# Performance work log

Hardware: AMD Instinct MI355X
Metric: run time of the kernel (lower is better)

## Reference

```python
import jax, jax.numpy as jnp
import numpy as np
from jax import lax

B, CIN, COUT, K, S, P, H, W = 8, 128, 256, 3, 1, 1, 64, 64


def setup_inputs() -> dict:
    key = jax.random.key(0)
    k1, k2, k3, k4, k5 = jax.random.split(key, 5)
    fan_off = CIN * K * K
    fan_dc = CIN * K * K
    return {
        "x": jax.random.normal(k1, (B, CIN, H, W), dtype=jnp.float32),
        # offset-predicting conv: Conv2d(CIN, 2*K*K, K, S, P, padding_mode='reflect')
        "w_off": jax.random.normal(k2, (2 * K * K, CIN, K, K), dtype=jnp.float32) / np.sqrt(fan_off),
        "b_off": jax.random.normal(k3, (2 * K * K,), dtype=jnp.float32) * 0.01,
        # deformable conv weights: DeformConv2d(CIN, COUT, K, S, P)
        "w_dc": jax.random.normal(k4, (COUT, CIN, K, K), dtype=jnp.float32) / np.sqrt(fan_dc),
        "b_dc": jax.random.normal(k5, (COUT,), dtype=jnp.float32) * 0.01,
    }


def _reflect_conv(x, w, b, stride, pad):
    # Conv2d with reflect padding
    xp = jnp.pad(x, ((0, 0), (0, 0), (pad, pad), (pad, pad)), mode="reflect")
    y = lax.conv_general_dilated(xp, w, (stride, stride), "VALID",
                                 dimension_numbers=("NCHW", "OIHW", "NCHW"))
    return y + b[None, :, None, None]


def _deform_conv(x, offset, w, b, k, stride, pad):
    # torchvision DeformConv2d (v1, no mask, 1 offset group)
    Bn, C, Hi, Wi = x.shape
    Ho, Wo = offset.shape[2], offset.shape[3]
    KK = k * k
    # offset layout: [B, 2*KK, Ho, Wo], interleaved (dy, dx) per kernel position
    off = offset.reshape(Bn, KK, 2, Ho, Wo)
    hb = jnp.arange(Ho, dtype=x.dtype) * stride - pad          # base rows
    wb = jnp.arange(Wo, dtype=x.dtype) * stride - pad          # base cols
    ki, kj = jnp.meshgrid(jnp.arange(k, dtype=x.dtype), jnp.arange(k, dtype=x.dtype), indexing="ij")
    ki, kj = ki.reshape(KK), kj.reshape(KK)
    # sampling locations [B, KK, Ho, Wo]
    py = off[:, :, 0] + hb[None, None, :, None] + ki[None, :, None, None]
    px = off[:, :, 1] + wb[None, None, None, :] + kj[None, :, None, None]
    y0 = jnp.floor(py)
    x0 = jnp.floor(px)
    dy = (py - y0).reshape(Bn, 1, -1)
    dx = (px - x0).reshape(Bn, 1, -1)
    y0i = y0.astype(jnp.int32)
    x0i = x0.astype(jnp.int32)
    xf = x.reshape(Bn, C, Hi * Wi)

    def gather(yi, xi):
        valid = (yi >= 0) & (yi < Hi) & (xi >= 0) & (xi < Wi)
        yc = jnp.clip(yi, 0, Hi - 1)
        xc = jnp.clip(xi, 0, Wi - 1)
        idx = (yc * Wi + xc).reshape(Bn, -1)                   # [B, KK*Ho*Wo]
        g = jax.vmap(lambda xb, ib: xb[:, ib])(xf, idx)        # [B, C, KK*Ho*Wo]
        return g * valid.reshape(Bn, 1, -1).astype(x.dtype)

    v00 = gather(y0i, x0i)
    v01 = gather(y0i, x0i + 1)
    v10 = gather(y0i + 1, x0i)
    v11 = gather(y0i + 1, x0i + 1)
    vals = (v00 * (1 - dy) * (1 - dx) + v01 * (1 - dy) * dx
            + v10 * dy * (1 - dx) + v11 * dy * dx)             # [B, C, KK*Ho*Wo]
    cols = vals.reshape(Bn, C, KK, Ho * Wo)
    out = jnp.einsum("bckl,ock->bol", cols, w.reshape(-1, C, KK))
    out = out + b[None, :, None]
    return out.reshape(Bn, -1, Ho, Wo)


def reference(x, w_off, b_off, w_dc, b_dc):
    x_offset = _reflect_conv(x, w_off, b_off, S, P)            # [B, 2*K*K, Ho, Wo]
    # torch.chunk followed by torch.concat is an identity on the offset tensor
    return _deform_conv(x, x_offset, w_dc, b_dc, K, S, P)
```

## Files before the change

### kernel.cpp

```cpp
#include <hip/hip_runtime.h>
#include <hip/hip_fp16.h>

typedef unsigned short u16;
typedef unsigned int   u32;
typedef u32   u32x2  __attribute__((ext_vector_type(2)));
typedef u32   u32x4  __attribute__((ext_vector_type(4)));
typedef short short8 __attribute__((ext_vector_type(8)));
typedef float f32x4  __attribute__((ext_vector_type(4)));
typedef _Float16 half8 __attribute__((ext_vector_type(8)));

__device__ __forceinline__ u16 f2h(float f) { return __half_as_ushort(__float2half(f)); }
__device__ __forceinline__ f32x4 mfma16(short8 a, short8 b, f32x4 c) {
  return __builtin_amdgcn_mfma_f32_16x16x32_f16(
      __builtin_bit_cast(half8, a), __builtin_bit_cast(half8, b), c, 0, 0, 0);
}
__device__ __forceinline__ __half2 h2cast(u32 u) { return __builtin_bit_cast(__half2, u); }

__global__ __launch_bounds__(256) void prep_fused(const float* __restrict__ x,
                                                  const float* __restrict__ w_dc,
                                                  const float* __restrict__ w_off,
                                                  u16* __restrict__ xh,
                                                  u16* __restrict__ Wl2,
                                                  u16* __restrict__ Wol2) {
  int bid = blockIdx.x;
  int tid = threadIdx.x;
  if (bid < 512) {
    __shared__ float tile[128][65];
    int swz = (bid & 7) * 64 + (bid >> 3);
    int b = swz >> 6, h = swz & 63;
    for (int i = 0; i < 32; ++i) {
      int c = (tid >> 6) + i * 4;
      int w = tid & 63;
      tile[c][w] = x[(((size_t)b * 128 + c) * 64 + h) * 64 + w];
    }
    __syncthreads();
    u16* dst = xh + ((size_t)(b * 64 + h) * 64) * 128;
    for (int j = 0; j < 32; ++j) {
      int c = tid & 127;
      int w = (tid >> 7) + 2 * j;
      dst[w * 128 + c] = f2h(tile[c][w]);
    }
  } else {
    int idx = (bid - 512) * 256 + tid;
    if (idx < 294912) {
      int e = idx & 7, lane = (idx >> 3) & 63, ks = (idx >> 9) & 3;
      int mt = (idx >> 11) & 15, kk = idx >> 15;
      int o = mt * 16 + (lane & 15), c = ks * 32 + (lane >> 4) * 8 + e;
      Wl2[idx] = f2h(w_dc[(o * 128 + c) * 9 + kk]);
    } else {
      int i2 = idx - 294912;
      int e = i2 & 7, lane = (i2 >> 3) & 63, ks = (i2 >> 9) & 3;
      int mt = (i2 >> 11) & 1, kk = i2 >> 12;
      int co = mt * 16 + (lane & 15), c = ks * 32 + (lane >> 4) * 8 + e;
      Wol2[i2] = (co < 18) ? f2h(w_off[(co * 128 + c) * 9 + kk]) : (u16)0;
    }
  }
}

__device__ __forceinline__ void make_entry_lds(u32x4* __restrict__ tbl, int kk,
                                               int ho, int wo, float offy, float offx) {
  int ki = kk / 3, kj = kk - ki * 3;
  float py = offy + (float)(ho + ki - 1);
  float px = offx + (float)(wo + kj - 1);
  float fy0 = floorf(py), fx0 = floorf(px);
  int y0 = (int)fy0, x0 = (int)fx0;
  float fy = py - fy0, fx = px - fx0;
  float w11 = fy * fx, w10 = fy - w11, w01 = fx - w11, w00 = 1.f - fy - fx + w11;
  bool iy0 = (y0 >= 0) & (y0 < 64), iy1 = (y0 >= -1) & (y0 < 63);
  bool ix0 = (x0 >= 0) & (x0 < 64), ix1 = (x0 >= -1) & (x0 < 63);
  int y0c = min(max(y0, 0), 63), x0c = min(max(x0, 0), 63);
  u32 addr00 = (u32)((y0c * 64 + x0c) * 128);
  u32 dx = (x0 >= 0 && x0 < 63) ? 128u : 0u;
  u32 dy = (y0 >= 0 && y0 < 63) ? 8192u : 0u;
  u32 wA = (u32)f2h((iy0 && ix0) ? w00 : 0.f) | ((u32)f2h((iy0 && ix1) ? w01 : 0.f) << 16);
  u32 wB = (u32)f2h((iy1 && ix0) ? w10 : 0.f) | ((u32)f2h((iy1 && ix1) ? w11 : 0.f) << 16);
  u32x4 ent; ent.x = addr00; ent.y = dx | (dy << 16); ent.z = wA; ent.w = wB;
  tbl[kk * 64 + wo] = ent;
}

__global__ __launch_bounds__(512, 4) void deform_fused(
    const u16* __restrict__ xh, const u16* __restrict__ Wl2,
    const u16* __restrict__ Wol2, const float* __restrict__ b_off,
    const float* __restrict__ b_dc, float* __restrict__ out) {
  __shared__ u16 cols[2][64][128];
  __shared__ u32x4 tbl[576];
  int bid = blockIdx.x;
  int swz = (bid & 7) * 64 + (bid >> 3);
  int b = swz >> 6, ho = swz & 63;
  int tid = threadIdx.x, lane = tid & 63, wv = tid >> 6;
  int ln15 = lane & 15, kg = lane >> 4;
  const u16* xb = xh + (size_t)b * 524288;

  int tl0 = tid >> 4;
  int tcl = (tid & 15) * 8;
  int swzc = tcl ^ ((tl0 & 7) << 3);

  u32x4 sv[2];
  auto stage_issue = [&](int kn) {
    int ki = kn / 3, kj = kn - ki * 3;
    int hr = ho + ki - 1; hr = hr < 0 ? -hr : (hr > 63 ? 126 - hr : hr);
#pragma unroll
    for (int i = 0; i < 2; ++i) {
      int l = tl0 + i * 32;
      int wr = l + kj - 1; wr = wr < 0 ? -wr : (wr > 63 ? 126 - wr : wr);
      sv[i] = *(const u32x4*)(xb + (hr * 64 + wr) * 128 + tcl);
    }
  };
  auto stage_write = [&](int dbuf) {
    *(u32x4*)&cols[dbuf][tl0][swzc]      = sv[0];
    *(u32x4*)&cols[dbuf][tl0 + 32][swzc] = sv[1];
  };

  int mt = wv & 1, ntq = wv >> 1;
  int lq = ntq * 16 + ln15;
  int swzb = (lq & 7) << 3;
  f32x4 oacc = {0.f, 0.f, 0.f, 0.f};

  stage_issue(0);
  stage_write(0);
  __syncthreads();
  for (int kk = 0; kk < 9; ++kk) {
    int buf = kk & 1;
    const u16* wb = Wol2 + ((kk * 2 + mt) * 4) * 512 + lane * 8;
    short8 a0 = *(const short8*)(wb);
    short8 a1 = *(const short8*)(wb + 512);
    short8 a2 = *(const short8*)(wb + 1024);
    short8 a3 = *(const short8*)(wb + 1536);
    if (kk < 8) stage_issue(kk + 1);
    oacc = mfma16(a0, *(const short8*)&cols[buf][lq][(0 * 32 + kg * 8) ^ swzb], oacc);
    oacc = mfma16(a1, *(const short8*)&cols[buf][lq][(1 * 32 + kg * 8) ^ swzb], oacc);
    oacc = mfma16(a2, *(const short8*)&cols[buf][lq][(2 * 32 + kg * 8) ^ swzb], oacc);
    oacc = mfma16(a3, *(const short8*)&cols[buf][lq][(3 * 32 + kg * 8) ^ swzb], oacc);
    if (kk < 8) stage_write(buf ^ 1);
    __syncthreads();
  }
  {
    int wo = lq;
    if (mt == 0) {
      int kkA = 2 * kg, kkB = 2 * kg + 1;
      make_entry_lds(tbl, kkA, ho, wo, oacc[0] + b_off[2 * kkA], oacc[1] + b_off[2 * kkA + 1]);
      make_entry_lds(tbl, kkB, ho, wo, oacc[2] + b_off[2 * kkB], oacc[3] + b_off[2 * kkB + 1]);
    } else if (kg == 0) {
      make_entry_lds(tbl, 8, ho, wo, oacc[0] + b_off[16], oacc[1] + b_off[17]);
    }
  }
  __syncthreads();

  u32x4 gv[2][4];
  u32x4 ge[2];
  auto gissue = [&](int g) {
#pragma unroll
    for (int i = 0; i < 2; ++i) {
      int l = tl0 + i * 32;
      u32x4 e = tbl[g * 64 + l];
      ge[i] = e;
      const u16* p = xb + e.x + tcl;
      u32 dxv = e.y & 0xffffu, dyv = e.y >> 16;
      gv[i][0] = *(const u32x4*)p;
      gv[i][1] = *(const u32x4*)(p + dxv);
      gv[i][2] = *(const u32x4*)(p + dyv);
      gv[i][3] = *(const u32x4*)(p + dyv + dxv);
    }
  };
  auto gwrite = [&](int dbuf) {
#pragma unroll
    for (int i = 0; i < 2; ++i) {
      __half2 wA = h2cast(ge[i].z), wB = h2cast(ge[i].w);
      __half2 w00 = __half2half2(wA.x), w01 = __half2half2(wA.y);
      __half2 w10 = __half2half2(wB.x), w11 = __half2half2(wB.y);
      u32x4 pv;
#pragma unroll
      for (int wd = 0; wd < 4; ++wd) {
        __half2 r = __hmul2(h2cast(gv[i][0][wd]), w00);
        r = __hfma2(h2cast(gv[i][1][wd]), w01, r);
        r = __hfma2(h2cast(gv[i][2][wd]), w10, r);
        r = __hfma2(h2cast(gv[i][3][wd]), w11, r);
        pv[wd] = __builtin_bit_cast(u32, r);
      }
      *(u32x4*)&cols[dbuf][tl0 + i * 32][swzc] = pv;
    }
  };

  f32x4 acc[2][4];
#pragma unroll
  for (int m = 0; m < 2; ++m)
#pragma unroll
    for (int n = 0; n < 4; ++n) acc[m][n] = (f32x4){0.f, 0.f, 0.f, 0.f};

  gissue(0);
  gwrite(0);
  __syncthreads();

  for (int kk = 0; kk < 9; ++kk) {
    int buf = kk & 1;
    const u16* wbase = Wl2 + (size_t)((kk * 16 + wv * 2) * 4) * 512;
    short8 a[8];
#pragma unroll
    for (int ks = 0; ks < 4; ++ks) {
      a[ks]     = *(const short8*)(wbase + ks * 512 + lane * 8);
      a[4 + ks] = *(const short8*)(wbase + (4 + ks) * 512 + lane * 8);
    }
    if (kk < 8) gissue(kk + 1);
#pragma unroll
    for (int ks = 0; ks < 4; ++ks) {
#pragma unroll
      for (int nt = 0; nt < 4; ++nt) {
        int l = nt * 16 + ln15;
        short8 bfv = *(const short8*)&cols[buf][l][(ks * 32 + kg * 8) ^ ((l & 7) << 3)];
        acc[0][nt] = mfma16(a[ks], bfv, acc[0][nt]);
        acc[1][nt] = mfma16(a[4 + ks], bfv, acc[1][nt]);
      }
    }
    if (kk < 8) gwrite(buf ^ 1);
    __syncthreads();
  }

#pragma unroll
  for (int mtt = 0; mtt < 2; ++mtt) {
#pragma unroll
    for (int r = 0; r < 4; ++r) {
      int o = wv * 32 + mtt * 16 + kg * 4 + r;
      float bias = b_dc[o];
      size_t base = ((size_t)(b * 256 + o)) * 4096 + ho * 64;
#pragma unroll
      for (int nt = 0; nt < 4; ++nt) {
        out[base + nt * 16 + ln15] = acc[mtt][nt][r] + bias;
      }
    }
  }
}

extern "C" void kernel_launch(void* const* d_in, const int* in_sizes, int n_in,
                              void* d_out, int out_size, void* d_ws, size_t ws_size,
                              hipStream_t stream) {
  const float* x     = (const float*)d_in[0];
  const float* w_off = (const float*)d_in[1];
  const float* b_off = (const float*)d_in[2];
  const float* w_dc  = (const float*)d_in[3];
  const float* b_dc  = (const float*)d_in[4];
  float* out = (float*)d_out;
  char* ws = (char*)d_ws;
  u16* xh   = (u16*)ws;
  u16* Wl2  = (u16*)(ws + 8388608);
  u16* Wol2 = (u16*)(ws + 8388608 + 589824);
  prep_fused  <<<dim3(1808), dim3(256), 0, stream>>>(x, w_dc, w_off, xh, Wl2, Wol2);
  deform_fused<<<dim3(512),  dim3(512), 0, stream>>>(xh, Wl2, Wol2, b_off, b_dc, out);
}
```

Measured before the change: 48.96 us.

## Stage three input rows once for offset conv and add MFMA priority hints

The offset-predicting conv now loads the three reflected input rows (3x64x128 halves) into shared memory in a single pass and indexes them per kernel tap with column reflection. This replaces nine double-buffered staging rounds, each with its own barrier. The shared slab is unioned with the cols/tbl buffers of the deformable phase, so the LDS footprint stays about the same. s_setprio is raised around the MFMA loops to favour matrix issue over other waves. The cost is more up-front load latency before any compute can start, with no overlap.

```diff
diff --git a/kernel.cpp b/kernel.cpp
--- a/kernel.cpp
+++ b/kernel.cpp
@@ -82,8 +82,11 @@
     const u16* __restrict__ xh, const u16* __restrict__ Wl2,
     const u16* __restrict__ Wol2, const float* __restrict__ b_off,
     const float* __restrict__ b_dc, float* __restrict__ out) {
-  __shared__ u16 cols[2][64][128];
-  __shared__ u32x4 tbl[576];
+  union SMU {
+    u16 slab[3][64][128];
+    struct { u16 cols[2][64][128]; u32x4 tbl[576]; } pb;
+  };
+  __shared__ SMU sm;
   int bid = blockIdx.x;
   int swz = (bid & 7) * 64 + (bid >> 3);
   int b = swz >> 6, ho = swz & 63;
@@ -95,53 +98,52 @@
   int tcl = (tid & 15) * 8;
   int swzc = tcl ^ ((tl0 & 7) << 3);
 
-  u32x4 sv[2];
-  auto stage_issue = [&](int kn) {
-    int ki = kn / 3, kj = kn - ki * 3;
-    int hr = ho + ki - 1; hr = hr < 0 ? -hr : (hr > 63 ? 126 - hr : hr);
-#pragma unroll
-    for (int i = 0; i < 2; ++i) {
-      int l = tl0 + i * 32;
-      int wr = l + kj - 1; wr = wr < 0 ? -wr : (wr > 63 ? 126 - wr : wr);
-      sv[i] = *(const u32x4*)(xb + (hr * 64 + wr) * 128 + tcl);
-    }
-  };
-  auto stage_write = [&](int dbuf) {
-    *(u32x4*)&cols[dbuf][tl0][swzc]      = sv[0];
-    *(u32x4*)&cols[dbuf][tl0 + 32][swzc] = sv[1];
-  };
+  {
+    u32x4 st[6];
+#pragma unroll
+    for (int i = 0; i < 6; ++i) {
+      int T = tid + i * 512;
+      int r = T >> 10, w = (T >> 4) & 63, cb = (T & 15) * 8;
+      int hr = ho + r - 1; hr = hr < 0 ? -hr : (hr > 63 ? 126 - hr : hr);
+      st[i] = *(const u32x4*)(xb + (hr * 64 + w) * 128 + cb);
+    }
+#pragma unroll
+    for (int i = 0; i < 6; ++i) {
+      int T = tid + i * 512;
+      int r = T >> 10, w = (T >> 4) & 63, cb = (T & 15) * 8;
+      *(u32x4*)&sm.slab[r][w][cb ^ ((w & 7) << 3)] = st[i];
+    }
+  }
+  __syncthreads();
 
   int mt = wv & 1, ntq = wv >> 1;
   int lq = ntq * 16 + ln15;
-  int swzb = (lq & 7) << 3;
   f32x4 oacc = {0.f, 0.f, 0.f, 0.f};
-
-  stage_issue(0);
-  stage_write(0);
-  __syncthreads();
+  __builtin_amdgcn_s_setprio(1);
+#pragma unroll
   for (int kk = 0; kk < 9; ++kk) {
-    int buf = kk & 1;
+    int ki = kk / 3, kj = kk - ki * 3;
+    int wr = lq + kj - 1; wr = wr < 0 ? -wr : (wr > 63 ? 126 - wr : wr);
     const u16* wb = Wol2 + ((kk * 2 + mt) * 4) * 512 + lane * 8;
-    short8 a0 = *(const short8*)(wb);
-    short8 a1 = *(const short8*)(wb + 512);
-    short8 a2 = *(const short8*)(wb + 1024);
-    short8 a3 = *(const short8*)(wb + 1536);
-    if (kk < 8) stage_issue(kk + 1);
-    oacc = mfma16(a0, *(const short8*)&cols[buf][lq][(0 * 32 + kg * 8) ^ swzb], oacc);
-    oacc = mfma16(a1, *(const short8*)&cols[buf][lq][(1 * 32 + kg * 8) ^ swzb], oacc);
-    oacc = mfma16(a2, *(const short8*)&cols[buf][lq][(2 * 32 + kg * 8) ^ swzb], oacc);
-    oacc = mfma16(a3, *(const short8*)&cols[buf][lq][(3 * 32 + kg * 8) ^ swzb], oacc);
-    if (kk < 8) stage_write(buf ^ 1);
-    __syncthreads();
-  }
+    int sb = (wr & 7) << 3;
+#pragma unroll
+    for (int ks = 0; ks < 4; ++ks) {
+      short8 af = *(const short8*)(wb + ks * 512);
+      short8 bf = *(const short8*)&sm.slab[ki][wr][(ks * 32 + kg * 8) ^ sb];
+      oacc = mfma16(af, bf, oacc);
+    }
+  }
+  __builtin_amdgcn_s_setprio(0);
+  __syncthreads();
+
   {
     int wo = lq;
     if (mt == 0) {
       int kkA = 2 * kg, kkB = 2 * kg + 1;
-      make_entry_lds(tbl, kkA, ho, wo, oacc[0] + b_off[2 * kkA], oacc[1] + b_off[2 * kkA + 1]);
-      make_entry_lds(tbl, kkB, ho, wo, oacc[2] + b_off[2 * kkB], oacc[3] + b_off[2 * kkB + 1]);
+      make_entry_lds(sm.pb.tbl, kkA, ho, wo, oacc[0] + b_off[2 * kkA], oacc[1] + b_off[2 * kkA + 1]);
+      make_entry_lds(sm.pb.tbl, kkB, ho, wo, oacc[2] + b_off[2 * kkB], oacc[3] + b_off[2 * kkB + 1]);
     } else if (kg == 0) {
-      make_entry_lds(tbl, 8, ho, wo, oacc[0] + b_off[16], oacc[1] + b_off[17]);
+      make_entry_lds(sm.pb.tbl, 8, ho, wo, oacc[0] + b_off[16], oacc[1] + b_off[17]);
     }
   }
   __syncthreads();
@@ -152,7 +154,7 @@
 #pragma unroll
     for (int i = 0; i < 2; ++i) {
       int l = tl0 + i * 32;
-      u32x4 e = tbl[g * 64 + l];
+      u32x4 e = sm.pb.tbl[g * 64 + l];
       ge[i] = e;
       const u16* p = xb + e.x + tcl;
       u32 dxv = e.y & 0xffffu, dyv = e.y >> 16;
@@ -177,7 +179,7 @@
         r = __hfma2(h2cast(gv[i][3][wd]), w11, r);
         pv[wd] = __builtin_bit_cast(u32, r);
       }
-      *(u32x4*)&cols[dbuf][tl0 + i * 32][swzc] = pv;
+      *(u32x4*)&sm.pb.cols[dbuf][tl0 + i * 32][swzc] = pv;
     }
   };
 
@@ -201,16 +203,18 @@
       a[4 + ks] = *(const short8*)(wbase + (4 + ks) * 512 + lane * 8);
     }
     if (kk < 8) gissue(kk + 1);
+    __builtin_amdgcn_s_setprio(1);
 #pragma unroll
     for (int ks = 0; ks < 4; ++ks) {
 #pragma unroll
       for (int nt = 0; nt < 4; ++nt) {
         int l = nt * 16 + ln15;
-        short8 bfv = *(const short8*)&cols[buf][l][(ks * 32 + kg * 8) ^ ((l & 7) << 3)];
+        short8 bfv = *(const short8*)&sm.pb.cols[buf][l][(ks * 32 + kg * 8) ^ ((l & 7) << 3)];
         acc[0][nt] = mfma16(a[ks], bfv, acc[0][nt]);
         acc[1][nt] = mfma16(a[4 + ks], bfv, acc[1][nt]);
       }
     }
+    __builtin_amdgcn_s_setprio(0);
     if (kk < 8) gwrite(buf ^ 1);
     __syncthreads();
   }
```

Result: faster. 47.61 us (-2.8%).
